# Kernel optimization log

Hardware: AMD Instinct MI355X
Metric: run time of the kernel (lower is better)

The kernel has to match this reference:

```python
import jax, jax.numpy as jnp
import numpy as np

NEG_SLOPE = 0.01  # F.leaky_relu default

def setup_inputs() -> dict:
    key = jax.random.key(0)
    ks = jax.random.split(key, 5)
    N, in_dim, out_dim = 8192, 256, 256
    x = jax.random.normal(ks[0], (N, in_dim), dtype=jnp.float32)
    W_fc = jax.random.normal(ks[1], (in_dim, out_dim), dtype=jnp.float32) / np.sqrt(in_dim)
    b_fc = jnp.zeros((out_dim,), dtype=jnp.float32)
    # attn_fc weight [2*out_dim] split into the two halves acting on h_i and h_j
    a1 = jax.random.normal(ks[2], (out_dim,), dtype=jnp.float32) / np.sqrt(2 * out_dim)
    a2 = jax.random.normal(ks[3], (out_dim,), dtype=jnp.float32) / np.sqrt(2 * out_dim)
    a_b = jnp.zeros((), dtype=jnp.float32)
    return {"x": x, "W_fc": W_fc, "b_fc": b_fc, "a1": a1, "a2": a2, "a_b": a_b}

def reference(x, W_fc, b_fc, a1, a2, a_b):
    # h = fc(x)
    h = x @ W_fc + b_fc                       # [N, out_dim]
    # attn_fc(cat[h_i, h_j]) == h_i.a1 + h_j.a2 + a_b (exact decomposition of the Linear)
    s1 = h @ a1                               # [N]
    s2 = h @ a2                               # [N]
    e = jax.nn.leaky_relu(s1[:, None] + s2[None, :] + a_b, NEG_SLOPE)  # [N, N]
    attention = jax.nn.softmax(e, axis=1)     # row-softmax over neighbors j
    return attention @ h                      # [N, out_dim]
```

## Files before the change

### kernel.cpp

```cpp
#include <hip/hip_runtime.h>
#include <math.h>


#define NN 8192
#define DD 256
#define NB 8192
#define CH 512
#define POS (NN / CH)
#define RANGE 8.0f
#define SCALE (NB / (2.0f * RANGE))
#define NEG_SLOPE 0.01f

__device__ __forceinline__ int bucket_of(float v) {
    v = fminf(fmaxf(v, -RANGE), RANGE);
    int b = (int)floorf((v + RANGE) * SCALE);
    if (b < 0) b = 0;
    if (b > NB - 1) b = NB - 1;
    return b;
}

__global__ __launch_bounds__(256) void ka_gemm(
    const float* __restrict__ x, const float* __restrict__ W,
    const float* __restrict__ bfc, const float* __restrict__ a1,
    const float* __restrict__ a2,
    float* __restrict__ h, float* __restrict__ s1, float* __restrict__ s2,
    int* __restrict__ cnt)
{
    const int t = threadIdx.x;
    const int ct = t & 63;
    const int rt = t >> 6;
    const int row0 = blockIdx.x * 16;
    __shared__ float xs[16][DD];

#pragma unroll
    for (int i = 0; i < 4; ++i) {
        const int f = i * 256 + t;
        const int r = f >> 6, c4 = f & 63;
        *reinterpret_cast<float4*>(&xs[r][c4 * 4]) =
            *reinterpret_cast<const float4*>(&x[(size_t)(row0 + r) * DD + c4 * 4]);
    }
    __syncthreads();

    float acc[4][4];
#pragma unroll
    for (int r = 0; r < 4; ++r)
#pragma unroll
        for (int c = 0; c < 4; ++c) acc[r][c] = 0.f;

#pragma unroll 2
    for (int k4 = 0; k4 < DD / 4; ++k4) {
        float4 wv[4];
#pragma unroll
        for (int kk = 0; kk < 4; ++kk)
            wv[kk] = *reinterpret_cast<const float4*>(&W[(size_t)(k4 * 4 + kk) * DD + ct * 4]);
        float4 xr[4];
#pragma unroll
        for (int r = 0; r < 4; ++r)
            xr[r] = *reinterpret_cast<const float4*>(&xs[rt * 4 + r][k4 * 4]);
#pragma unroll
        for (int kk = 0; kk < 4; ++kk) {
#pragma unroll
            for (int r = 0; r < 4; ++r) {
                const float xv = (kk == 0) ? xr[r].x : (kk == 1) ? xr[r].y : (kk == 2) ? xr[r].z : xr[r].w;
                acc[r][0] = fmaf(xv, wv[kk].x, acc[r][0]);
                acc[r][1] = fmaf(xv, wv[kk].y, acc[r][1]);
                acc[r][2] = fmaf(xv, wv[kk].z, acc[r][2]);
                acc[r][3] = fmaf(xv, wv[kk].w, acc[r][3]);
            }
        }
    }

    const float4 bv  = *reinterpret_cast<const float4*>(&bfc[ct * 4]);
    const float4 a1v = *reinterpret_cast<const float4*>(&a1[ct * 4]);
    const float4 a2v = *reinterpret_cast<const float4*>(&a2[ct * 4]);
    const int lane = t & 63;

#pragma unroll
    for (int r = 0; r < 4; ++r) {
        acc[r][0] += bv.x; acc[r][1] += bv.y; acc[r][2] += bv.z; acc[r][3] += bv.w;
        const int row = row0 + rt * 4 + r;
        float4 hv = make_float4(acc[r][0], acc[r][1], acc[r][2], acc[r][3]);
        *reinterpret_cast<float4*>(&h[(size_t)row * DD + ct * 4]) = hv;
        float v1 = acc[r][0] * a1v.x + acc[r][1] * a1v.y + acc[r][2] * a1v.z + acc[r][3] * a1v.w;
        float v2 = acc[r][0] * a2v.x + acc[r][1] * a2v.y + acc[r][2] * a2v.z + acc[r][3] * a2v.w;
#pragma unroll
        for (int off = 32; off; off >>= 1) {
            v1 += __shfl_xor(v1, off, 64);
            v2 += __shfl_xor(v2, off, 64);
        }
        if (lane == 0) {
            s1[row] = v1;
            s2[row] = v2;
            atomicAdd(&cnt[bucket_of(v2)], 1);
        }
    }
}

__global__ __launch_bounds__(256) void kb_scan(int* __restrict__ cnt, int* __restrict__ boff)
{
    __shared__ int lds[256];
    const int t = threadIdx.x;
    const int base = t * 32;
    int loc[32];
    int s = 0;
#pragma unroll
    for (int k = 0; k < 32; ++k) { loc[k] = s; s += cnt[base + k]; }
    lds[t] = s;
    __syncthreads();
    for (int off = 1; off < 256; off <<= 1) {
        const int v = (t >= off) ? lds[t - off] : 0;
        __syncthreads();
        lds[t] += v;
        __syncthreads();
    }
    const int excl = (t > 0) ? lds[t - 1] : 0;
#pragma unroll
    for (int k = 0; k < 32; ++k) {
        const int val = excl + loc[k];
        boff[base + k] = val;
        cnt[base + k] = val;
    }
    if (t == 0) boff[NB] = NN;
}

__global__ __launch_bounds__(256) void kc_scatter(
    const float* __restrict__ s2, int* __restrict__ cursor, int* __restrict__ perm)
{
    const int j = blockIdx.x * blockDim.x + threadIdx.x;
    if (j < NN) {
        const int b = bucket_of(s2[j]);
        const int p = atomicAdd(&cursor[b], 1);
        perm[p] = j;
    }
}

__global__ __launch_bounds__(256) void kc2_rank(
    const float* __restrict__ s2, const int* __restrict__ perm,
    const int* __restrict__ boff, int* __restrict__ perm2, float* __restrict__ s2s)
{
    const int j = blockIdx.x * blockDim.x + threadIdx.x;
    if (j < NN) {
        const float v = s2[j];
        const int bk = bucket_of(v);
        const int p0 = boff[bk], p1 = boff[bk + 1];
        int rank = 0;
        for (int p = p0; p < p1; ++p) {
            const int k = perm[p];
            const float vk = s2[k];
            rank += (vk < v) || (vk == v && k < j);
        }
        const int pos = p0 + rank;
        perm2[pos] = j;
        s2s[pos] = v;
    }
}

__global__ __launch_bounds__(256) void kd1_tot(
    const float* __restrict__ h, const int* __restrict__ perm2,
    const float* __restrict__ s2s,
    float* __restrict__ TE, float* __restrict__ TF,
    float* __restrict__ sTE, float* __restrict__ sTF)
{
    const int w = threadIdx.x >> 6, lane = threadIdx.x & 63;
    const int c = blockIdx.x * 4 + w;
    const int p0 = c * POS;
    float vE[POS], vF[POS];
    int jj[POS];
#pragma unroll
    for (int k = 0; k < POS; ++k) {
        const float v = s2s[p0 + k];
        vE[k] = expf(v);
        vF[k] = expf(NEG_SLOPE * v);
        jj[k] = perm2[p0 + k];
    }
    float4 te = make_float4(0.f, 0.f, 0.f, 0.f);
    float4 tf = make_float4(0.f, 0.f, 0.f, 0.f);
#pragma unroll
    for (int k = 0; k < POS; ++k) {
        const float4 hv = *reinterpret_cast<const float4*>(&h[(size_t)jj[k] * DD + lane * 4]);
        te.x = fmaf(vE[k], hv.x, te.x); te.y = fmaf(vE[k], hv.y, te.y);
        te.z = fmaf(vE[k], hv.z, te.z); te.w = fmaf(vE[k], hv.w, te.w);
        tf.x = fmaf(vF[k], hv.x, tf.x); tf.y = fmaf(vF[k], hv.y, tf.y);
        tf.z = fmaf(vF[k], hv.z, tf.z); tf.w = fmaf(vF[k], hv.w, tf.w);
    }
    *reinterpret_cast<float4*>(&TE[(size_t)c * DD + lane * 4]) = te;
    *reinterpret_cast<float4*>(&TF[(size_t)c * DD + lane * 4]) = tf;
    if (lane == 0) {
        float se = 0.f, sf = 0.f;
#pragma unroll
        for (int k = 0; k < POS; ++k) { se += vE[k]; sf += vF[k]; }
        sTE[c] = se; sTF[c] = sf;
    }
}

__device__ __forceinline__ void scan512_excl(float* lds, float* tmp, int t)
{
    const float a0 = lds[2 * t], a1 = lds[2 * t + 1];
    tmp[t] = a0 + a1;
    __syncthreads();
    for (int off = 1; off < 256; off <<= 1) {
        const float v = (t >= off) ? tmp[t - off] : 0.f;
        __syncthreads();
        tmp[t] += v;
        __syncthreads();
    }
    const float base = (t > 0) ? tmp[t - 1] : 0.f;
    lds[2 * t] = base;
    lds[2 * t + 1] = base + a0;
    __syncthreads();
}

__global__ __launch_bounds__(256) void kd2_scan(
    float* __restrict__ TE, float* __restrict__ TF,
    float* __restrict__ sTE, float* __restrict__ sTF)
{
    const int t = threadIdx.x;
    const int b = blockIdx.x;
    __shared__ float lds[CH];
    __shared__ float tmp[256];
    const int q0 = 2 * t, q1 = 2 * t + 1;

    if (b < 256) {
        const int d = b;
        lds[q0] = TE[(size_t)(511 - q0) * DD + d];
        lds[q1] = TE[(size_t)(511 - q1) * DD + d];
        __syncthreads();
        scan512_excl(lds, tmp, t);
        TE[(size_t)(511 - q0) * DD + d] = lds[q0];
        TE[(size_t)(511 - q1) * DD + d] = lds[q1];
        if (t == 0) TE[(size_t)CH * DD + d] = 0.f;
    } else if (b < 512) {
        const int d = b - 256;
        lds[q0] = TF[(size_t)q0 * DD + d];
        lds[q1] = TF[(size_t)q1 * DD + d];
        __syncthreads();
        scan512_excl(lds, tmp, t);
        TF[(size_t)q0 * DD + d] = lds[q0];
        TF[(size_t)q1 * DD + d] = lds[q1];
        if (t == 0) TF[(size_t)CH * DD + d] = tmp[255];
    } else {
        lds[q0] = sTE[511 - q0]; lds[q1] = sTE[511 - q1];
        __syncthreads();
        scan512_excl(lds, tmp, t);
        sTE[511 - q0] = lds[q0]; sTE[511 - q1] = lds[q1];
        if (t == 0) sTE[CH] = 0.f;
        __syncthreads();
        lds[q0] = sTF[q0]; lds[q1] = sTF[q1];
        __syncthreads();
        scan512_excl(lds, tmp, t);
        sTF[q0] = lds[q0]; sTF[q1] = lds[q1];
        if (t == 0) sTF[CH] = tmp[255];
    }
}

__global__ __launch_bounds__(256) void ke_out(
    const float* __restrict__ h, const float* __restrict__ s1,
    const float* __restrict__ s2s, const int* __restrict__ perm2,
    const float* __restrict__ TE, const float* __restrict__ TF,
    const float* __restrict__ sTE, const float* __restrict__ sTF,
    const float* __restrict__ ab, float* __restrict__ out)
{
    const int w = threadIdx.x >> 6, lane = threadIdx.x & 63;
    const int i = blockIdx.x * 4 + w;
    const float c = s1[i] + ab[0];
    const float tau = -c;
    const float A = expf(c);
    const float Alo = expf(NEG_SLOPE * c);

    int lo = 0, hi = NN;
    while (lo < hi) {
        const int mid = (lo + hi) >> 1;
        const bool lt = (s2s[mid] < tau);
        lo = lt ? (mid + 1) : lo;
        hi = lt ? hi : mid;
    }
    const int c0 = lo >> 4;
    const int m = lo & 15;

    float4 numE = *reinterpret_cast<const float4*>(&TE[(size_t)c0 * DD + lane * 4]);
    float4 numF = *reinterpret_cast<const float4*>(&TF[(size_t)c0 * DD + lane * 4]);
    float denE = sTE[c0];
    float denF = sTF[c0];

    if (c0 < CH) {
        const int p0 = c0 * POS;
#pragma unroll
        for (int k = 0; k < POS; ++k) {
            const float v = s2s[p0 + k];
            const int j = perm2[p0 + k];
            const float4 hv = *reinterpret_cast<const float4*>(&h[(size_t)j * DD + lane * 4]);
            if (k >= m) {
                const float e = expf(v);
                numE.x = fmaf(e, hv.x, numE.x); numE.y = fmaf(e, hv.y, numE.y);
                numE.z = fmaf(e, hv.z, numE.z); numE.w = fmaf(e, hv.w, numE.w);
                denE += e;
            } else {
                const float f = expf(NEG_SLOPE * v);
                numF.x = fmaf(f, hv.x, numF.x); numF.y = fmaf(f, hv.y, numF.y);
                numF.z = fmaf(f, hv.z, numF.z); numF.w = fmaf(f, hv.w, numF.w);
                denF += f;
            }
        }
    }

    const float inv = 1.f / fmaf(A, denE, Alo * denF);
    float4 o;
    o.x = fmaf(A, numE.x, Alo * numF.x) * inv;
    o.y = fmaf(A, numE.y, Alo * numF.y) * inv;
    o.z = fmaf(A, numE.z, Alo * numF.z) * inv;
    o.w = fmaf(A, numE.w, Alo * numF.w) * inv;
    *reinterpret_cast<float4*>(&out[(size_t)i * DD + lane * 4]) = o;
}

extern "C" void kernel_launch(void* const* d_in, const int* in_sizes, int n_in,
                              void* d_out, int out_size, void* d_ws, size_t ws_size,
                              hipStream_t stream)
{
    const float* x   = (const float*)d_in[0];
    const float* W   = (const float*)d_in[1];
    const float* bfc = (const float*)d_in[2];
    const float* a1  = (const float*)d_in[3];
    const float* a2  = (const float*)d_in[4];
    const float* ab  = (const float*)d_in[5];
    float* out = (float*)d_out;

    float* h    = (float*)d_ws;
    float* TE   = h + (size_t)NN * DD;
    float* TF   = TE + (size_t)(CH + 1) * DD;
    float* s1   = TF + (size_t)(CH + 1) * DD;
    float* s2   = s1 + NN;
    float* s2s  = s2 + NN;
    float* sTE  = s2s + NN;
    float* sTF  = sTE + (CH + 1);
    int* cnt    = (int*)(sTF + (CH + 1));
    int* boff   = cnt + NB;
    int* perm   = boff + (NB + 1);
    int* perm2  = perm + NN;

    hipMemsetAsync(cnt, 0, NB * sizeof(int), stream);
    ka_gemm <<<NN / 16, 256, 0, stream>>>(x, W, bfc, a1, a2, h, s1, s2, cnt);
    kb_scan <<<1, 256, 0, stream>>>(cnt, boff);
    kc_scatter<<<NN / 256, 256, 0, stream>>>(s2, cnt, perm);
    kc2_rank<<<NN / 256, 256, 0, stream>>>(s2, perm, boff, perm2, s2s);
    kd1_tot <<<CH / 4, 256, 0, stream>>>(h, perm2, s2s, TE, TF, sTE, sTF);
    kd2_scan<<<513, 256, 0, stream>>>(TE, TF, sTE, sTF);
    ke_out  <<<NN / 4, 256, 0, stream>>>(h, s1, s2s, perm2, TE, TF, sTE, sTF, ab, out);
}
```

Baseline: 142.9 us.

## Fuse histogram, scan, scatter and rank into one single-block LDS sort kernel

Replaces the global-atomic bucket histogram, the scan kernel, the scatter kernel and the rank kernel with one single-workgroup kernel that keeps the histogram and offsets in shared memory. It also drops the memset and the atomics from the GEMM epilogue. The aim is to remove several launches and the global atomic traffic. In exchange, all of the sorting work now runs on a single compute unit with serial strided loops.

```diff
diff --git a/kernel.cpp b/kernel.cpp
--- a/kernel.cpp
+++ b/kernel.cpp
@@ -23,8 +23,7 @@
     const float* __restrict__ x, const float* __restrict__ W,
     const float* __restrict__ bfc, const float* __restrict__ a1,
     const float* __restrict__ a2,
-    float* __restrict__ h, float* __restrict__ s1, float* __restrict__ s2,
-    int* __restrict__ cnt)
+    float* __restrict__ h, float* __restrict__ s1, float* __restrict__ s2)
 {
     const int t = threadIdx.x;
     const int ct = t & 63;
@@ -91,58 +90,61 @@
         if (lane == 0) {
             s1[row] = v1;
             s2[row] = v2;
-            atomicAdd(&cnt[bucket_of(v2)], 1);
-        }
-    }
-}
-
-__global__ __launch_bounds__(256) void kb_scan(int* __restrict__ cnt, int* __restrict__ boff)
-{
-    __shared__ int lds[256];
+        }
+    }
+}
+
+__global__ __launch_bounds__(256) void ksort(
+    const float* __restrict__ s2, int* __restrict__ perm,
+    int* __restrict__ perm2, float* __restrict__ s2s)
+{
+    __shared__ int A[NB];
+    __shared__ unsigned short B[NB + 1];
+    __shared__ int temp[256];
     const int t = threadIdx.x;
-    const int base = t * 32;
-    int loc[32];
-    int s = 0;
-#pragma unroll
-    for (int k = 0; k < 32; ++k) { loc[k] = s; s += cnt[base + k]; }
-    lds[t] = s;
-    __syncthreads();
-    for (int off = 1; off < 256; off <<= 1) {
-        const int v = (t >= off) ? lds[t - off] : 0;
-        __syncthreads();
-        lds[t] += v;
-        __syncthreads();
-    }
-    const int excl = (t > 0) ? lds[t - 1] : 0;
-#pragma unroll
-    for (int k = 0; k < 32; ++k) {
-        const int val = excl + loc[k];
-        boff[base + k] = val;
-        cnt[base + k] = val;
-    }
-    if (t == 0) boff[NB] = NN;
-}
-
-__global__ __launch_bounds__(256) void kc_scatter(
-    const float* __restrict__ s2, int* __restrict__ cursor, int* __restrict__ perm)
-{
-    const int j = blockIdx.x * blockDim.x + threadIdx.x;
-    if (j < NN) {
-        const int b = bucket_of(s2[j]);
-        const int p = atomicAdd(&cursor[b], 1);
+
+    for (int k = t; k < NB; k += 256) A[k] = 0;
+    __syncthreads();
+
+    for (int j = t; j < NN; j += 256) atomicAdd(&A[bucket_of(s2[j])], 1);
+    __syncthreads();
+
+    {
+        const int base = t * 32;
+        int loc[32];
+        int s = 0;
+#pragma unroll
+        for (int k = 0; k < 32; ++k) { loc[k] = s; s += A[base + k]; }
+        temp[t] = s;
+        __syncthreads();
+        for (int off = 1; off < 256; off <<= 1) {
+            const int v = (t >= off) ? temp[t - off] : 0;
+            __syncthreads();
+            temp[t] += v;
+            __syncthreads();
+        }
+        const int excl = (t > 0) ? temp[t - 1] : 0;
+#pragma unroll
+        for (int k = 0; k < 32; ++k) {
+            const int val = excl + loc[k];
+            A[base + k] = val;
+            B[base + k] = (unsigned short)val;
+        }
+        if (t == 0) B[NB] = (unsigned short)NN;
+    }
+    __syncthreads();
+
+    for (int j = t; j < NN; j += 256) {
+        const int bk = bucket_of(s2[j]);
+        const int p = atomicAdd(&A[bk], 1);
         perm[p] = j;
     }
-}
-
-__global__ __launch_bounds__(256) void kc2_rank(
-    const float* __restrict__ s2, const int* __restrict__ perm,
-    const int* __restrict__ boff, int* __restrict__ perm2, float* __restrict__ s2s)
-{
-    const int j = blockIdx.x * blockDim.x + threadIdx.x;
-    if (j < NN) {
+    __syncthreads();
+
+    for (int j = t; j < NN; j += 256) {
         const float v = s2[j];
         const int bk = bucket_of(v);
-        const int p0 = boff[bk], p1 = boff[bk + 1];
+        const int p0 = B[bk], p1 = B[bk + 1];
         int rank = 0;
         for (int p = p0; p < p1; ++p) {
             const int k = perm[p];
@@ -332,16 +334,11 @@
     float* s2s  = s2 + NN;
     float* sTE  = s2s + NN;
     float* sTF  = sTE + (CH + 1);
-    int* cnt    = (int*)(sTF + (CH + 1));
-    int* boff   = cnt + NB;
-    int* perm   = boff + (NB + 1);
+    int* perm   = (int*)(sTF + (CH + 1));
     int* perm2  = perm + NN;
 
-    hipMemsetAsync(cnt, 0, NB * sizeof(int), stream);
-    ka_gemm <<<NN / 16, 256, 0, stream>>>(x, W, bfc, a1, a2, h, s1, s2, cnt);
-    kb_scan <<<1, 256, 0, stream>>>(cnt, boff);
-    kc_scatter<<<NN / 256, 256, 0, stream>>>(s2, cnt, perm);
-    kc2_rank<<<NN / 256, 256, 0, stream>>>(s2, perm, boff, perm2, s2s);
+    ka_gemm <<<NN / 16, 256, 0, stream>>>(x, W, bfc, a1, a2, h, s1, s2);
+    ksort   <<<1, 256, 0, stream>>>(s2, perm, perm2, s2s);
     kd1_tot <<<CH / 4, 256, 0, stream>>>(h, perm2, s2s, TE, TF, sTE, sTF);
     kd2_scan<<<513, 256, 0, stream>>>(TE, TF, sTE, sTF);
     ke_out  <<<NN / 4, 256, 0, stream>>>(h, s1, s2s, perm2, TE, TF, sTE, sTF, ab, out);
```

After: 244.0 us. 70.8% more time.
